# Optimization experiments

Measured on AMD Instinct MI355X. Metric: run time of the kernel, lower is better.

The kernel has to match this reference:

```python
import jax, jax.numpy as jnp
import numpy as np

B, S, D = 8, 4096, 1024
MINR, MAXR = 0.9, 0.999


def setup_inputs() -> dict:
    key = jax.random.key(0)
    ks = jax.random.split(key, 10)

    def dense(k, fin, fout):
        # lecun_normal-style init for flax nn.Dense kernels
        return jax.random.normal(k, (fin, fout), jnp.float32) * (fin ** -0.5)

    x = jax.random.normal(ks[0], (B, S, D), jnp.float32)
    # RNN 'a' param: stable_init -> uniform in [min_rad, max_rad]
    a_fwd = jax.random.uniform(ks[1], (D,), jnp.float32, MINR, MAXR)
    # RGLRU 'a' param: recurrence_init
    u = jax.random.uniform(ks[2], (D,), jnp.float32)
    log_rad = 0.5 * jnp.log(u * (MAXR ** 2 - MINR ** 2) + MINR ** 2)
    a_param = jnp.log(jnp.exp(-log_rad) - 1.0)
    return {
        "x": x,
        "a_fwd": a_fwd,
        "Wf1": dense(ks[3], D, D), "bf1": jnp.zeros((D,), jnp.float32),
        "Wf2": dense(ks[4], D, D), "bf2": jnp.zeros((D,), jnp.float32),
        "Wbx": dense(ks[5], D, D), "bbx": jnp.zeros((D,), jnp.float32),
        "Wgx": dense(ks[6], D, D), "bgx": jnp.zeros((D,), jnp.float32),
        "Wga": dense(ks[7], D, D), "bga": jnp.zeros((D,), jnp.float32),
        "a_param": a_param,
        "Wb2": dense(ks[8], D, D), "bb2": jnp.zeros((D,), jnp.float32),
    }


def reference(x, a_fwd, Wf1, bf1, Wf2, bf2, Wbx, bbx, Wgx, bgx, Wga, bga,
              a_param, Wb2, bb2):
    b = x.shape[0]
    d = Wf1.shape[1]
    identity = x
    xg = jax.nn.gelu(x)  # flax nn.gelu default = tanh approximation

    # ---- forward branch: plain linear RNN  h = a*h + x_t ----
    u = xg @ Wf1 + bf1                       # [B,S,D]
    u_sf = jnp.swapaxes(u, 0, 1)             # [S,B,D]

    def step_f(h, ut):
        h = a_fwd * h + ut
        return h, h

    _, hf = jax.lax.scan(step_f, jnp.zeros((b, d), u.dtype), u_sf)
    out_f = jnp.swapaxes(hf, 0, 1) @ Wf2 + bf2

    # ---- backward branch: RG-LRU, reversed scan ----
    v = xg @ Wbx + bbx                       # [B,S,D]
    gate_x = jax.nn.sigmoid(v @ Wgx + bgx)
    gate_a = jax.nn.sigmoid(v @ Wga + bga)
    log_a = -8.0 * gate_a * jax.nn.softplus(a_param)
    a = jnp.exp(log_a)                       # [B,S,D]
    # h = a*h + sqrt(1 - a^2) * (gate_x * v)
    scaled_in = jnp.sqrt(1.0 - jnp.exp(2.0 * log_a)) * (gate_x * v)

    a_sf = jnp.swapaxes(a, 0, 1)             # [S,B,D]
    in_sf = jnp.swapaxes(scaled_in, 0, 1)    # [S,B,D]

    def step_b(h, inp):
        a_t, g_t = inp
        h = a_t * h + g_t
        return h, h

    _, hb = jax.lax.scan(step_b, jnp.zeros((b, d), v.dtype), (a_sf, in_sf),
                         reverse=True)
    out_b = jnp.swapaxes(hb, 0, 1) @ Wb2 + bb2

    return out_f + out_b + identity
```

## Files before the change

kernel.cpp:

```cpp
#include <hip/hip_runtime.h>

typedef __bf16 bf16;
typedef __bf16 bf16x8 __attribute__((ext_vector_type(8)));
typedef float floatx4 __attribute__((ext_vector_type(4)));

typedef __attribute__((address_space(1))) const void gvoid_t;
typedef __attribute__((address_space(3))) void lvoid_t;

#define B_DIM 8
#define S_DIM 4096
#define M_DIM 32768
#define CHUNK 128
#define NCHUNK 32

__device__ __forceinline__ void gload_lds16(const bf16* g, bf16* l) {
    __builtin_amdgcn_global_load_lds((gvoid_t*)g, (lvoid_t*)l, 16, 0, 0);
}

__device__ __forceinline__ float gelu_tanh(float x) {
    float x3 = x * x * x;
    return 0.5f * x * (1.0f + tanhf(0.7978845608028654f * (x + 0.044715f * x3)));
}

__device__ __forceinline__ float sigmoidf(float z) {
    return 1.0f / (1.0f + expf(-z));
}

__global__ void prep_weights(const float* __restrict__ W0, const float* __restrict__ W1,
                             const float* __restrict__ W2, const float* __restrict__ W3,
                             const float* __restrict__ W4, const float* __restrict__ W5,
                             bf16* __restrict__ T0, bf16* __restrict__ T1,
                             bf16* __restrict__ T2, bf16* __restrict__ T3,
                             bf16* __restrict__ T4, bf16* __restrict__ T5) {
    __shared__ float tile[32][33];
    int mz = blockIdx.z;
    const float* W = mz == 0 ? W0 : mz == 1 ? W1 : mz == 2 ? W2 : mz == 3 ? W3 : mz == 4 ? W4 : W5;
    bf16* T = mz == 0 ? T0 : mz == 1 ? T1 : mz == 2 ? T2 : mz == 3 ? T3 : mz == 4 ? T4 : T5;
    int tn = blockIdx.x * 32;
    int tk = blockIdx.y * 32;
    int tx = threadIdx.x & 31, ty = threadIdx.x >> 5;
#pragma unroll
    for (int i = 0; i < 4; ++i)
        tile[ty + i * 8][tx] = W[(size_t)(tk + ty + i * 8) * 1024 + tn + tx];
    __syncthreads();
#pragma unroll
    for (int i = 0; i < 4; ++i)
        T[(size_t)(tn + ty + i * 8) * 1024 + tk + tx] = (bf16)tile[tx][ty + i * 8];
}

__global__ void sp_kernel(const float* __restrict__ a_param, float* __restrict__ spbuf) {
    int d = blockIdx.x * 256 + threadIdx.x;
    spbuf[d] = log1pf(expf(a_param[d]));
}

__global__ void gelu_kernel(const float* __restrict__ x, bf16* __restrict__ xg) {
    size_t i = (size_t)blockIdx.x * 256 + threadIdx.x;
    float4 v = ((const float4*)x)[i];
    bf16 o0 = (bf16)gelu_tanh(v.x), o1 = (bf16)gelu_tanh(v.y);
    bf16 o2 = (bf16)gelu_tanh(v.z), o3 = (bf16)gelu_tanh(v.w);
    typedef __bf16 bf16x4 __attribute__((ext_vector_type(4)));
    bf16x4 o = {o0, o1, o2, o3};
    ((bf16x4*)xg)[i] = o;
}

template <int MODE>
__launch_bounds__(256, 2)
__global__ void gemm_k1024(const bf16* __restrict__ A, const bf16* __restrict__ Bt,
                           float* __restrict__ outf, bf16* __restrict__ outh,
                           const float* __restrict__ bias,
                           const float* __restrict__ auxf,
                           const bf16* __restrict__ labuf,
                           const bf16* __restrict__ vbuf) {
    __shared__ __align__(16) bf16 lsA[128 * 64];
    __shared__ __align__(16) bf16 lsB[128 * 64];
    const int tid = threadIdx.x;
    const int wave = tid >> 6;
    const int lane = tid & 63;
    const int lane15 = lane & 15;
    const int quad = lane >> 4;
    const int wm = wave & 1, wn = wave >> 1;
    const int blk = blockIdx.x;
    const int xcd = blk & 7;
    const int j = blk >> 3;
    const long m0 = (long)(xcd * 32 + (j >> 3)) * 128;
    const long n0 = (long)(j & 7) * 128;
    const int r_in = lane >> 3;
    const int cch = lane & 7;

    floatx4 acc[4][4] = {};

    for (int kt = 0; kt < 16; ++kt) {
        __syncthreads();
#pragma unroll
        for (int i = 0; i < 4; ++i) {
            int rr = (i * 4 + wave) * 8 + r_in;
            int g = cch ^ (rr & 7);
            gload_lds16(A + (size_t)(m0 + rr) * 1024 + kt * 64 + g * 8, &lsA[(i * 4 + wave) * 512]);
            gload_lds16(Bt + (size_t)(n0 + rr) * 1024 + kt * 64 + g * 8, &lsB[(i * 4 + wave) * 512]);
        }
        __syncthreads();
#pragma unroll
        for (int kk = 0; kk < 2; ++kk) {
            bf16x8 af[4], bfr[4];
#pragma unroll
            for (int mi = 0; mi < 4; ++mi) {
                int ml = wm * 64 + mi * 16 + lane15;
                af[mi] = *(const bf16x8*)&lsA[ml * 64 + ((kk * 4 + quad) ^ (ml & 7)) * 8];
            }
#pragma unroll
            for (int ni = 0; ni < 4; ++ni) {
                int nl = wn * 64 + ni * 16 + lane15;
                bfr[ni] = *(const bf16x8*)&lsB[nl * 64 + ((kk * 4 + quad) ^ (nl & 7)) * 8];
            }
#pragma unroll
            for (int mi = 0; mi < 4; ++mi)
#pragma unroll
                for (int ni = 0; ni < 4; ++ni)
                    acc[mi][ni] = __builtin_amdgcn_mfma_f32_16x16x32_bf16(af[mi], bfr[ni], acc[mi][ni], 0, 0, 0);
        }
    }

#pragma unroll
    for (int mi = 0; mi < 4; ++mi) {
#pragma unroll
        for (int ni = 0; ni < 4; ++ni) {
            floatx4 v = acc[mi][ni];
            long gn = n0 + wn * 64 + ni * 16 + lane15;
#pragma unroll
            for (int r = 0; r < 4; ++r) {
                long gm = m0 + wm * 64 + mi * 16 + quad * 4 + r;
                size_t o = (size_t)gm * 1024 + gn;
                if (MODE == 0) {
                    outf[o] = v[r] + bias[gn];
                } else if (MODE == 1) {
                    outh[o] = (bf16)(v[r] + bias[gn]);
                } else if (MODE == 2) {
                    float z = v[r] + bias[gn];
                    outh[o] = (bf16)(-8.0f * sigmoidf(z) * auxf[gn]);
                } else {
                    float z = v[r] + bias[gn];
                    float laf = (float)labuf[o];
                    float sc = sqrtf(-expm1f(2.0f * laf)) * sigmoidf(z) * (float)vbuf[o];
                    outh[o] = (bf16)sc;
                }
            }
        }
    }
}

__launch_bounds__(256, 2)
__global__ void gemm_cat(const bf16* __restrict__ A0, const bf16* __restrict__ A1,
                         const bf16* __restrict__ B0t, const bf16* __restrict__ B1t,
                         float* __restrict__ outf,
                         const float* __restrict__ bias0, const float* __restrict__ bias1,
                         const float* __restrict__ xres) {
    __shared__ __align__(16) bf16 lsA[128 * 64];
    __shared__ __align__(16) bf16 lsB[128 * 64];
    const int tid = threadIdx.x;
    const int wave = tid >> 6;
    const int lane = tid & 63;
    const int lane15 = lane & 15;
    const int quad = lane >> 4;
    const int wm = wave & 1, wn = wave >> 1;
    const int blk = blockIdx.x;
    const int xcd = blk & 7;
    const int j = blk >> 3;
    const long m0 = (long)(xcd * 32 + (j >> 3)) * 128;
    const long n0 = (long)(j & 7) * 128;
    const int r_in = lane >> 3;
    const int cch = lane & 7;

    floatx4 acc[4][4] = {};

    for (int kt = 0; kt < 32; ++kt) {
        const bf16* Ap = (kt < 16) ? A0 : A1;
        const bf16* Bp = (kt < 16) ? B0t : B1t;
        const int ko = kt & 15;
        __syncthreads();
#pragma unroll
        for (int i = 0; i < 4; ++i) {
            int rr = (i * 4 + wave) * 8 + r_in;
            int g = cch ^ (rr & 7);
            gload_lds16(Ap + (size_t)(m0 + rr) * 1024 + ko * 64 + g * 8, &lsA[(i * 4 + wave) * 512]);
            gload_lds16(Bp + (size_t)(n0 + rr) * 1024 + ko * 64 + g * 8, &lsB[(i * 4 + wave) * 512]);
        }
        __syncthreads();
#pragma unroll
        for (int kk = 0; kk < 2; ++kk) {
            bf16x8 af[4], bfr[4];
#pragma unroll
            for (int mi = 0; mi < 4; ++mi) {
                int ml = wm * 64 + mi * 16 + lane15;
                af[mi] = *(const bf16x8*)&lsA[ml * 64 + ((kk * 4 + quad) ^ (ml & 7)) * 8];
            }
#pragma unroll
            for (int ni = 0; ni < 4; ++ni) {
                int nl = wn * 64 + ni * 16 + lane15;
                bfr[ni] = *(const bf16x8*)&lsB[nl * 64 + ((kk * 4 + quad) ^ (nl & 7)) * 8];
            }
#pragma unroll
            for (int mi = 0; mi < 4; ++mi)
#pragma unroll
                for (int ni = 0; ni < 4; ++ni)
                    acc[mi][ni] = __builtin_amdgcn_mfma_f32_16x16x32_bf16(af[mi], bfr[ni], acc[mi][ni], 0, 0, 0);
        }
    }

#pragma unroll
    for (int mi = 0; mi < 4; ++mi) {
#pragma unroll
        for (int ni = 0; ni < 4; ++ni) {
            floatx4 v = acc[mi][ni];
            long gn = n0 + wn * 64 + ni * 16 + lane15;
#pragma unroll
            for (int r = 0; r < 4; ++r) {
                long gm = m0 + wm * 64 + mi * 16 + quad * 4 + r;
                size_t o = (size_t)gm * 1024 + gn;
                outf[o] = v[r] + bias0[gn] + bias1[gn] + xres[o];
            }
        }
    }
}

__global__ void fscan1(const float* __restrict__ u, const float* __restrict__ a_fwd,
                       float* __restrict__ carry) {
    int d = (blockIdx.x & 3) * 256 + threadIdx.x;
    int c = (blockIdx.x >> 2) & 31;
    int b = blockIdx.x >> 7;
    float a = a_fwd[d];
    const float* up = u + ((size_t)(b * S_DIM + c * CHUNK)) * 1024 + d;
    float h = 0.0f;
#pragma unroll 8
    for (int t = 0; t < CHUNK; ++t) h = fmaf(a, h, up[(size_t)t * 1024]);
    carry[((size_t)c * 8 + b) * 1024 + d] = h;
}
__global__ void fscan2(const float* __restrict__ carry, const float* __restrict__ a_fwd,
                       float* __restrict__ H) {
    int idx = blockIdx.x * 256 + threadIdx.x;
    int d = idx & 1023, b = idx >> 10;
    float a = a_fwd[d];
    float aL = a;
#pragma unroll
    for (int i = 0; i < 7; ++i) aL *= aL;
    float h = 0.0f;
    for (int c = 0; c < NCHUNK; ++c) {
        size_t o = ((size_t)c * 8 + b) * 1024 + d;
        H[o] = h;
        h = fmaf(aL, h, carry[o]);
    }
}
__global__ void fscan3(const float* __restrict__ u, const float* __restrict__ a_fwd,
                       const float* __restrict__ H, bf16* __restrict__ hf) {
    int d = (blockIdx.x & 3) * 256 + threadIdx.x;
    int c = (blockIdx.x >> 2) & 31;
    int b = blockIdx.x >> 7;
    float a = a_fwd[d];
    const float* up = u + ((size_t)(b * S_DIM + c * CHUNK)) * 1024 + d;
    bf16* op = hf + ((size_t)(b * S_DIM + c * CHUNK)) * 1024 + d;
    float h = H[((size_t)c * 8 + b) * 1024 + d];
#pragma unroll 4
    for (int t = 0; t < CHUNK; ++t) {
        h = fmaf(a, h, up[(size_t)t * 1024]);
        op[(size_t)t * 1024] = (bf16)h;
    }
}

__global__ void bscan1(const bf16* __restrict__ la, const bf16* __restrict__ sc,
                       float* __restrict__ BL, float* __restrict__ BP) {
    int d = (blockIdx.x & 3) * 256 + threadIdx.x;
    int c = (blockIdx.x >> 2) & 31;
    int b = blockIdx.x >> 7;
    const bf16* lap = la + ((size_t)(b * S_DIM + c * CHUNK)) * 1024 + d;
    const bf16* gp = sc + ((size_t)(b * S_DIM + c * CHUNK)) * 1024 + d;
    float h = 0.0f, slog = 0.0f;
#pragma unroll 4
    for (int t = CHUNK - 1; t >= 0; --t) {
        float laf = (float)lap[(size_t)t * 1024];
        h = fmaf(expf(laf), h, (float)gp[(size_t)t * 1024]);
        slog += laf;
    }
    size_t o = ((size_t)c * 8 + b) * 1024 + d;
    BL[o] = h;
    BP[o] = expf(slog);
}
__global__ void bscan2(const float* __restrict__ BL, const float* __restrict__ BP,
                       float* __restrict__ R) {
    int idx = blockIdx.x * 256 + threadIdx.x;
    int d = idx & 1023, b = idx >> 10;
    float r = 0.0f;
    for (int c = NCHUNK - 1; c >= 0; --c) {
        size_t o = ((size_t)c * 8 + b) * 1024 + d;
        R[o] = r;
        r = fmaf(BP[o], r, BL[o]);
    }
}
__global__ void bscan3(const bf16* __restrict__ la, const bf16* __restrict__ sc,
                       const float* __restrict__ R, bf16* __restrict__ hb) {
    int d = (blockIdx.x & 3) * 256 + threadIdx.x;
    int c = (blockIdx.x >> 2) & 31;
    int b = blockIdx.x >> 7;
    const bf16* lap = la + ((size_t)(b * S_DIM + c * CHUNK)) * 1024 + d;
    const bf16* gp = sc + ((size_t)(b * S_DIM + c * CHUNK)) * 1024 + d;
    bf16* op = hb + ((size_t)(b * S_DIM + c * CHUNK)) * 1024 + d;
    float h = R[((size_t)c * 8 + b) * 1024 + d];
#pragma unroll 4
    for (int t = CHUNK - 1; t >= 0; --t) {
        h = fmaf(expf((float)lap[(size_t)t * 1024]), h, (float)gp[(size_t)t * 1024]);
        op[(size_t)t * 1024] = (bf16)h;
    }
}

extern "C" void kernel_launch(void* const* d_in, const int* in_sizes, int n_in,
                              void* d_out, int out_size, void* d_ws, size_t ws_size,
                              hipStream_t stream) {
    const float* x       = (const float*)d_in[0];
    const float* a_fwd   = (const float*)d_in[1];
    const float* Wf1     = (const float*)d_in[2];
    const float* bf1     = (const float*)d_in[3];
    const float* Wf2     = (const float*)d_in[4];
    const float* bf2     = (const float*)d_in[5];
    const float* Wbx     = (const float*)d_in[6];
    const float* bbx     = (const float*)d_in[7];
    const float* Wgx     = (const float*)d_in[8];
    const float* bgx     = (const float*)d_in[9];
    const float* Wga     = (const float*)d_in[10];
    const float* bga     = (const float*)d_in[11];
    const float* a_param = (const float*)d_in[12];
    const float* Wb2     = (const float*)d_in[13];
    const float* bb2     = (const float*)d_in[14];
    float* out = (float*)d_out;
    (void)in_sizes; (void)n_in; (void)out_size; (void)ws_size;

    char* ws = (char*)d_ws;
    size_t off = 0;
    const size_t WSZ = (size_t)1024 * 1024 * 2;
    bf16* Wf1t = (bf16*)(ws + off); off += WSZ;
    bf16* Wbxt = (bf16*)(ws + off); off += WSZ;
    bf16* Wgxt = (bf16*)(ws + off); off += WSZ;
    bf16* Wgat = (bf16*)(ws + off); off += WSZ;
    bf16* Wf2t = (bf16*)(ws + off); off += WSZ;
    bf16* Wb2t = (bf16*)(ws + off); off += WSZ;
    float* spbuf = (float*)(ws + off); off += 4096;
    const size_t BSZ = (size_t)M_DIM * 1024 * 2;
    bf16* buf0 = (bf16*)(ws + off); off += BSZ;
    bf16* buf1 = (bf16*)(ws + off); off += BSZ;
    bf16* buf2 = (bf16*)(ws + off); off += BSZ;
    float* Fc = (float*)(ws + off); off += (size_t)NCHUNK * 8 * 1024 * 4;
    float* FH = (float*)(ws + off); off += (size_t)NCHUNK * 8 * 1024 * 4;
    float* BL = (float*)(ws + off); off += (size_t)NCHUNK * 8 * 1024 * 4;
    float* BP = (float*)(ws + off); off += (size_t)NCHUNK * 8 * 1024 * 4;
    float* BR = (float*)(ws + off); off += (size_t)NCHUNK * 8 * 1024 * 4;

    bf16* xg = buf0;
    bf16* hf = buf0;
    bf16* vb = buf1;
    bf16* hb = buf1;
    bf16* la = buf2;
    float* u = (float*)d_out;
    bf16* sc = (bf16*)d_out;

    prep_weights<<<dim3(32, 32, 6), 256, 0, stream>>>(Wf1, Wbx, Wgx, Wga, Wf2, Wb2,
                                                      Wf1t, Wbxt, Wgxt, Wgat, Wf2t, Wb2t);
    sp_kernel<<<4, 256, 0, stream>>>(a_param, spbuf);
    gelu_kernel<<<32768, 256, 0, stream>>>(x, xg);
    gemm_k1024<0><<<2048, 256, 0, stream>>>(xg, Wf1t, u, nullptr, bf1, nullptr, nullptr, nullptr);
    gemm_k1024<1><<<2048, 256, 0, stream>>>(xg, Wbxt, nullptr, vb, bbx, nullptr, nullptr, nullptr);
    fscan1<<<1024, 256, 0, stream>>>(u, a_fwd, Fc);
    fscan2<<<32, 256, 0, stream>>>(Fc, a_fwd, FH);
    fscan3<<<1024, 256, 0, stream>>>(u, a_fwd, FH, hf);
    gemm_k1024<2><<<2048, 256, 0, stream>>>(vb, Wgat, nullptr, la, bga, spbuf, nullptr, nullptr);
    gemm_k1024<3><<<2048, 256, 0, stream>>>(vb, Wgxt, nullptr, sc, bgx, nullptr, la, vb);
    bscan1<<<1024, 256, 0, stream>>>(la, sc, BL, BP);
    bscan2<<<32, 256, 0, stream>>>(BL, BP, BR);
    bscan3<<<1024, 256, 0, stream>>>(la, sc, BR, hb);
    gemm_cat<<<2048, 256, 0, stream>>>(hf, hb, Wf2t, Wb2t, out, bf2, bb2, x);
}
```

Baseline: 916.2 us.

## Enlarge GEMM tiles to 128x256 with 8 waves per block

All GEMM kernels move from 128x128 tiles with 4 waves to 128x256 tiles with 8 waves (512 threads), halving the grid to 1024 blocks. Each thread now issues one global-to-LDS load per 64-row slab, with simplified addressing precomputed outside the k-loop. The larger N tile means each A row is loaded from global memory half as often, raising arithmetic intensity. In exchange LDS use per block grows to 48KB and the wave-to-tile mapping and block-to-tile mapping change.

```diff
diff --git a/kernel.cpp b/kernel.cpp
--- a/kernel.cpp
+++ b/kernel.cpp
@@ -64,53 +64,54 @@
 }
 
 template <int MODE>
-__launch_bounds__(256, 2)
-__global__ void gemm_k1024(const bf16* __restrict__ A, const bf16* __restrict__ Bt,
-                           float* __restrict__ outf, bf16* __restrict__ outh,
-                           const float* __restrict__ bias,
-                           const float* __restrict__ auxf,
-                           const bf16* __restrict__ labuf,
-                           const bf16* __restrict__ vbuf) {
-    __shared__ __align__(16) bf16 lsA[128 * 64];
-    __shared__ __align__(16) bf16 lsB[128 * 64];
+__launch_bounds__(512, 4)
+__global__ void gemm_w(const bf16* __restrict__ A, const bf16* __restrict__ Bt,
+                       float* __restrict__ outf, bf16* __restrict__ outh,
+                       const float* __restrict__ bias,
+                       const float* __restrict__ auxf,
+                       const bf16* __restrict__ labuf,
+                       const bf16* __restrict__ vbuf) {
+    __shared__ __align__(16) bf16 lsA[2][4096];
+    __shared__ __align__(16) bf16 lsB[4][4096];
     const int tid = threadIdx.x;
     const int wave = tid >> 6;
     const int lane = tid & 63;
     const int lane15 = lane & 15;
     const int quad = lane >> 4;
-    const int wm = wave & 1, wn = wave >> 1;
+    const int wm = wave >> 2;
+    const int wn = wave & 3;
     const int blk = blockIdx.x;
     const int xcd = blk & 7;
     const int j = blk >> 3;
-    const long m0 = (long)(xcd * 32 + (j >> 3)) * 128;
-    const long n0 = (long)(j & 7) * 128;
-    const int r_in = lane >> 3;
-    const int cch = lane & 7;
+    const long m0 = (long)(xcd * 32 + (j >> 2)) * 128;
+    const long n0 = (long)(j & 3) * 256;
+    const int sr = tid >> 3;
+    const int sk8 = (tid & 7) ^ (sr & 7);
+    const bf16* gA = A + (size_t)(m0 + sr) * 1024 + sk8 * 8;
+    const bf16* gB = Bt + (size_t)(n0 + sr) * 1024 + sk8 * 8;
 
     floatx4 acc[4][4] = {};
 
     for (int kt = 0; kt < 16; ++kt) {
         __syncthreads();
-#pragma unroll
-        for (int i = 0; i < 4; ++i) {
-            int rr = (i * 4 + wave) * 8 + r_in;
-            int g = cch ^ (rr & 7);
-            gload_lds16(A + (size_t)(m0 + rr) * 1024 + kt * 64 + g * 8, &lsA[(i * 4 + wave) * 512]);
-            gload_lds16(Bt + (size_t)(n0 + rr) * 1024 + kt * 64 + g * 8, &lsB[(i * 4 + wave) * 512]);
-        }
+        gload_lds16(gA + (size_t)kt * 64, &lsA[0][tid * 8]);
+        gload_lds16(gA + (size_t)64 * 1024 + kt * 64, &lsA[1][tid * 8]);
+#pragma unroll
+        for (int i = 0; i < 4; ++i)
+            gload_lds16(gB + (size_t)(i * 64) * 1024 + kt * 64, &lsB[i][tid * 8]);
         __syncthreads();
 #pragma unroll
         for (int kk = 0; kk < 2; ++kk) {
             bf16x8 af[4], bfr[4];
 #pragma unroll
             for (int mi = 0; mi < 4; ++mi) {
-                int ml = wm * 64 + mi * 16 + lane15;
-                af[mi] = *(const bf16x8*)&lsA[ml * 64 + ((kk * 4 + quad) ^ (ml & 7)) * 8];
+                int rl = mi * 16 + lane15;
+                af[mi] = *(const bf16x8*)&lsA[wm][rl * 64 + ((kk * 4 + quad) ^ (rl & 7)) * 8];
             }
 #pragma unroll
             for (int ni = 0; ni < 4; ++ni) {
-                int nl = wn * 64 + ni * 16 + lane15;
-                bfr[ni] = *(const bf16x8*)&lsB[nl * 64 + ((kk * 4 + quad) ^ (nl & 7)) * 8];
+                int rl = ni * 16 + lane15;
+                bfr[ni] = *(const bf16x8*)&lsB[wn][rl * 64 + ((kk * 4 + quad) ^ (rl & 7)) * 8];
             }
 #pragma unroll
             for (int mi = 0; mi < 4; ++mi)
@@ -148,27 +149,28 @@
     }
 }
 
-__launch_bounds__(256, 2)
+__launch_bounds__(512, 4)
 __global__ void gemm_cat(const bf16* __restrict__ A0, const bf16* __restrict__ A1,
                          const bf16* __restrict__ B0t, const bf16* __restrict__ B1t,
                          float* __restrict__ outf,
                          const float* __restrict__ bias0, const float* __restrict__ bias1,
                          const float* __restrict__ xres) {
-    __shared__ __align__(16) bf16 lsA[128 * 64];
-    __shared__ __align__(16) bf16 lsB[128 * 64];
+    __shared__ __align__(16) bf16 lsA[2][4096];
+    __shared__ __align__(16) bf16 lsB[4][4096];
     const int tid = threadIdx.x;
     const int wave = tid >> 6;
     const int lane = tid & 63;
     const int lane15 = lane & 15;
     const int quad = lane >> 4;
-    const int wm = wave & 1, wn = wave >> 1;
+    const int wm = wave >> 2;
+    const int wn = wave & 3;
     const int blk = blockIdx.x;
     const int xcd = blk & 7;
     const int j = blk >> 3;
-    const long m0 = (long)(xcd * 32 + (j >> 3)) * 128;
-    const long n0 = (long)(j & 7) * 128;
-    const int r_in = lane >> 3;
-    const int cch = lane & 7;
+    const long m0 = (long)(xcd * 32 + (j >> 2)) * 128;
+    const long n0 = (long)(j & 3) * 256;
+    const int sr = tid >> 3;
+    const int sk8 = (tid & 7) ^ (sr & 7);
 
     floatx4 acc[4][4] = {};
 
@@ -176,27 +178,27 @@
         const bf16* Ap = (kt < 16) ? A0 : A1;
         const bf16* Bp = (kt < 16) ? B0t : B1t;
         const int ko = kt & 15;
+        const bf16* gA = Ap + (size_t)(m0 + sr) * 1024 + sk8 * 8 + (size_t)ko * 64;
+        const bf16* gB = Bp + (size_t)(n0 + sr) * 1024 + sk8 * 8 + (size_t)ko * 64;
         __syncthreads();
-#pragma unroll
-        for (int i = 0; i < 4; ++i) {
-            int rr = (i * 4 + wave) * 8 + r_in;
-            int g = cch ^ (rr & 7);
-            gload_lds16(Ap + (size_t)(m0 + rr) * 1024 + ko * 64 + g * 8, &lsA[(i * 4 + wave) * 512]);
-            gload_lds16(Bp + (size_t)(n0 + rr) * 1024 + ko * 64 + g * 8, &lsB[(i * 4 + wave) * 512]);
-        }
+        gload_lds16(gA, &lsA[0][tid * 8]);
+        gload_lds16(gA + (size_t)64 * 1024, &lsA[1][tid * 8]);
+#pragma unroll
+        for (int i = 0; i < 4; ++i)
+            gload_lds16(gB + (size_t)(i * 64) * 1024, &lsB[i][tid * 8]);
         __syncthreads();
 #pragma unroll
         for (int kk = 0; kk < 2; ++kk) {
             bf16x8 af[4], bfr[4];
 #pragma unroll
             for (int mi = 0; mi < 4; ++mi) {
-                int ml = wm * 64 + mi * 16 + lane15;
-                af[mi] = *(const bf16x8*)&lsA[ml * 64 + ((kk * 4 + quad) ^ (ml & 7)) * 8];
+                int rl = mi * 16 + lane15;
+                af[mi] = *(const bf16x8*)&lsA[wm][rl * 64 + ((kk * 4 + quad) ^ (rl & 7)) * 8];
             }
 #pragma unroll
             for (int ni = 0; ni < 4; ++ni) {
-                int nl = wn * 64 + ni * 16 + lane15;
-                bfr[ni] = *(const bf16x8*)&lsB[nl * 64 + ((kk * 4 + quad) ^ (nl & 7)) * 8];
+                int rl = ni * 16 + lane15;
+                bfr[ni] = *(const bf16x8*)&lsB[wn][rl * 64 + ((kk * 4 + quad) ^ (rl & 7)) * 8];
             }
 #pragma unroll
             for (int mi = 0; mi < 4; ++mi)
@@ -363,15 +365,15 @@
                                                       Wf1t, Wbxt, Wgxt, Wgat, Wf2t, Wb2t);
     sp_kernel<<<4, 256, 0, stream>>>(a_param, spbuf);
     gelu_kernel<<<32768, 256, 0, stream>>>(x, xg);
-    gemm_k1024<0><<<2048, 256, 0, stream>>>(xg, Wf1t, u, nullptr, bf1, nullptr, nullptr, nullptr);
-    gemm_k1024<1><<<2048, 256, 0, stream>>>(xg, Wbxt, nullptr, vb, bbx, nullptr, nullptr, nullptr);
+    gemm_w<0><<<1024, 512, 0, stream>>>(xg, Wf1t, u, nullptr, bf1, nullptr, nullptr, nullptr);
+    gemm_w<1><<<1024, 512, 0, stream>>>(xg, Wbxt, nullptr, vb, bbx, nullptr, nullptr, nullptr);
     fscan1<<<1024, 256, 0, stream>>>(u, a_fwd, Fc);
     fscan2<<<32, 256, 0, stream>>>(Fc, a_fwd, FH);
     fscan3<<<1024, 256, 0, stream>>>(u, a_fwd, FH, hf);
-    gemm_k1024<2><<<2048, 256, 0, stream>>>(vb, Wgat, nullptr, la, bga, spbuf, nullptr, nullptr);
-    gemm_k1024<3><<<2048, 256, 0, stream>>>(vb, Wgxt, nullptr, sc, bgx, nullptr, la, vb);
+    gemm_w<2><<<1024, 512, 0, stream>>>(vb, Wgat, nullptr, la, bga, spbuf, nullptr, nullptr);
+    gemm_w<3><<<1024, 512, 0, stream>>>(vb, Wgxt, nullptr, sc, bgx, nullptr, la, vb);
     bscan1<<<1024, 256, 0, stream>>>(la, sc, BL, BP);
     bscan2<<<32, 256, 0, stream>>>(BL, BP, BR);
     bscan3<<<1024, 256, 0, stream>>>(la, sc, BR, hb);
-    gemm_cat<<<2048, 256, 0, stream>>>(hf, hb, Wf2t, Wb2t, out, bf2, bb2, x);
-}
+    gemm_cat<<<1024, 512, 0, stream>>>(hf, hb, Wf2t, Wb2t, out, bf2, bb2, x);
+}
```

New measurement: 906.4 us. No clear change (-1.1%).
